# Kernel optimization log

Measured on AMD Instinct MI355X. Metric: run time of the kernel, lower is better.

## Reference

```python
import jax, jax.numpy as jnp
import numpy as np

B, T, P, D, L = 16, 120, 96, 128, 2


def setup_inputs() -> dict:
    key = jax.random.key(0)
    k1, k2, k3, k4 = jax.random.split(key, 4)
    x = jax.random.normal(k1, (B, P, D, T), dtype=jnp.float32)
    # distances: symmetric-ish positive pairwise distances from random 3D points
    pts = jax.random.uniform(k2, (B, T, P, 3), dtype=jnp.float32) * 5.0
    diff = pts[:, :, :, None, :] - pts[:, :, None, :, :]
    distances = jnp.sqrt(jnp.sum(diff * diff, axis=-1) + 1e-12)
    # contiguous-prefix padding mask (matches the original self-loop loop semantics)
    counts = jax.random.randint(k3, (B,), P // 2, P + 1)
    padding_mask = jnp.arange(P)[None, :] < counts[:, None]
    # params: xavier_uniform with gain 1e-5 ~ tiny; bias 0; LN gamma=1, beta=0
    limit = 1e-5 * np.sqrt(6.0 / (D + D))
    W = jax.random.uniform(k4, (L, D, D), minval=-limit, maxval=limit, dtype=jnp.float32)
    b = jnp.zeros((L, D), dtype=jnp.float32)
    gamma = jnp.ones((L, D), dtype=jnp.float32)
    beta = jnp.zeros((L, D), dtype=jnp.float32)
    return {"x": x, "distances": distances, "padding_mask": padding_mask,
            "W": W, "b": b, "gamma": gamma, "beta": beta}


def _build_adjacency(distances, padding_mask):
    # valid_mask: [B,T,P,P]
    vm2d = (padding_mask[:, :, None] & padding_mask[:, None, :]).astype(distances.dtype)  # [B,P,P]
    vm = vm2d[:, None, :, :]
    vd = distances * vm
    pos = (vd > 0).astype(distances.dtype)
    n = jnp.sum(pos)
    mean = jnp.sum(vd * pos) / n
    var = jnp.sum(((vd - mean) ** 2) * pos) / (n - 1.0)  # unbiased, as torch.std
    sigma = jnp.sqrt(var) + 1e-8
    adj = jnp.exp(-(distances ** 2) / (2.0 * sigma ** 2)) * vm
    # self loops on valid (contiguous-prefix) nodes: add diag(mask)
    eye_mask = jnp.eye(P, dtype=distances.dtype)[None, :, :] * padding_mask[:, :, None].astype(distances.dtype)
    adj = adj + eye_mask[:, None, :, :]
    # symmetric normalization D^{-1/2} A D^{-1/2}
    deg = jnp.clip(jnp.sum(adj, axis=-1, keepdims=True), 1e-8, None)  # [B,T,P,1]
    deg = jnp.clip(deg * padding_mask[:, None, :, None].astype(distances.dtype), 1e-8, None)
    dis = deg ** -0.5
    adj = dis * adj * jnp.swapaxes(dis, -2, -1)
    return adj * vm


def _layer_norm_D(x, g, bt, eps=1e-5):
    # x: [B,P,D,T]; normalize over D axis
    mu = jnp.mean(x, axis=2, keepdims=True)
    var = jnp.mean((x - mu) ** 2, axis=2, keepdims=True)
    return (x - mu) * jax.lax.rsqrt(var + eps) * g[None, None, :, None] + bt[None, None, :, None]


def reference(x, distances, padding_mask, W, b, gamma, beta):
    adj = _build_adjacency(distances, padding_mask)  # [B,T,P,P]
    mask_f = padding_mask.astype(x.dtype)
    for l in range(L):
        xt = jnp.transpose(x, (0, 3, 1, 2))                      # [B,T,P,D]
        h = jnp.einsum('btpd,de->btpe', xt, W[l])                # x @ W
        o = jnp.einsum('btpq,btqd->btpd', adj, h)                # A @ xW
        o = jax.nn.relu(o + b[l])
        o = o * mask_f[:, None, :, None]
        o = jnp.transpose(o, (0, 2, 3, 1))                       # [B,P,D,T]
        o = _layer_norm_D(o, gamma[l], beta[l])
        x = x + o
    return x
```

## Files before the change

kernel.cpp:

```cpp
#include <hip/hip_runtime.h>
#include <math.h>

typedef __bf16 bf16_t;
typedef __bf16 bf16x8 __attribute__((ext_vector_type(8)));
typedef __bf16 bf16x4 __attribute__((ext_vector_type(4)));
typedef float f32x4 __attribute__((ext_vector_type(4)));

namespace {
constexpr int kB = 16;
constexpr int kT = 120;
constexpr int kP = 96;
constexpr int kD = 128;
constexpr int kBT = kB * kT;
constexpr int kPP = kP * kP;
constexpr int kPD = kP * kD;
constexpr long long kND = (long long)kBT * kPP;
constexpr unsigned kND4 = (unsigned)(kND / 4);

constexpr int PREP_BLOCKS = 128;
constexpr int TIN_TILES = (kPD / 64) * kB;
constexpr int TILES_PER_BLOCK = 3;
constexpr int TIN_BLOCKS = TIN_TILES / TILES_PER_BLOCK;
constexpr int STATS_BLOCKS = 2048;
constexpr int FRONT_BLOCKS = PREP_BLOCKS + TIN_BLOCKS + STATS_BLOCKS;

constexpr int YS = 136;
constexpr int HS = 104;
constexpr int OS = 132;
constexpr int AS = 104;
constexpr int HT_OFF = 26112;
constexpr int AL_OFF = 52736;
constexpr int MROW_OFF = 72704;
constexpr int DIS_OFF = 73088;
constexpr int SMEM_B = 73472;
}

__device__ __forceinline__ f32x4 mfma16(bf16x8 a, bf16x8 b, f32x4 c) {
    return __builtin_amdgcn_mfma_f32_16x16x32_bf16(a, b, c, 0, 0, 0);
}

__global__ __launch_bounds__(256) void k_front(const float* __restrict__ x,
                                               bf16_t* __restrict__ y,
                                               const float* __restrict__ dist,
                                               const unsigned char* __restrict__ mraw,
                                               int* __restrict__ mask,
                                               double* __restrict__ stats,
                                               const float* __restrict__ W,
                                               bf16_t* __restrict__ wT) {
    __shared__ __align__(16) char sm[30976];
    const int bid = blockIdx.x;
    const int tid = threadIdx.x;

    if (bid < PREP_BLOCKS) {
        int pb = bid;
        int l = pb >> 6;
        int idx = (pb & 63) * 256 + tid;
        int n = idx >> 7, k = idx & 127;
        wT[l * 16384 + n * 128 + k] = (bf16_t)W[l * 16384 + k * 128 + n];

        if (pb == 0) {
            const unsigned int* u32 = (const unsigned int*)mraw;
            unsigned int w0 = u32[0];
            int mode;
            if (w0 == 0x01010101u) mode = 0;
            else if (w0 == 1u) mode = 1;
            else mode = 2;
            for (int i = tid; i < kB * kP; i += 256) {
                int v;
                if (mode == 0)      v = (mraw[i] != 0);
                else if (mode == 1) v = (u32[i] != 0);
                else                v = (((const float*)mraw)[i] != 0.0f);
                mask[i] = v;
            }
        }
    } else if (bid < PREP_BLOCKS + TIN_BLOCKS) {
        float* tile = (float*)sm;
        int tb = bid - PREP_BLOCKS;
        int tile0 = tb * TILES_PER_BLOCK;

        float4 pf[8];
        {
            const float* xb = x + (long long)tile0 * 7680;
            #pragma unroll
            for (int k = 0; k < 8; ++k) {
                int idx = k * 256 + tid;
                if (idx < 1920) pf[k] = *(const float4*)(xb + idx * 4);
            }
        }

        for (int it = 0; it < TILES_PER_BLOCK; ++it) {
            int tg = tile0 + it;
            #pragma unroll
            for (int k = 0; k < 8; ++k) {
                int idx = k * 256 + tid;
                if (idx < 1920) {
                    int r = idx / 30, c = (idx - r * 30) * 4;
                    tile[r * 121 + c + 0] = pf[k].x;
                    tile[r * 121 + c + 1] = pf[k].y;
                    tile[r * 121 + c + 2] = pf[k].z;
                    tile[r * 121 + c + 3] = pf[k].w;
                }
            }
            __syncthreads();
            if (it + 1 < TILES_PER_BLOCK) {
                const float* xb = x + (long long)(tg + 1) * 7680;
                #pragma unroll
                for (int k = 0; k < 8; ++k) {
                    int idx = k * 256 + tid;
                    if (idx < 1920) pf[k] = *(const float4*)(xb + idx * 4);
                }
            }
            int b = tg / (kPD / 64);
            int pd0 = (tg - b * (kPD / 64)) * 64;
            bf16_t* yb = y + (long long)b * kT * kPD + pd0;
            #pragma unroll
            for (int k = 0; k < 4; ++k) {
                int idx = k * 256 + tid;
                if (idx < 960) {
                    int t = idx >> 3, dg = idx & 7;
                    bf16x8 o;
                    #pragma unroll
                    for (int j = 0; j < 8; ++j) o[j] = (bf16_t)tile[(dg * 8 + j) * 121 + t];
                    *(bf16x8*)(yb + (long long)t * kPD + dg * 8) = o;
                }
            }
            __syncthreads();
        }
    } else {
        int sb = bid - PREP_BLOCKS - TIN_BLOCKS;
        int* ml = (int*)sm;
        double* sh = (double*)(sm + 6144);
        {
            const unsigned int* u32 = (const unsigned int*)mraw;
            unsigned int w0 = u32[0];
            int mode;
            if (w0 == 0x01010101u) mode = 0;
            else if (w0 == 1u) mode = 1;
            else mode = 2;
            for (int i = tid; i < kB * kP; i += 256) {
                int v;
                if (mode == 0)      v = (mraw[i] != 0);
                else if (mode == 1) v = (u32[i] != 0);
                else                v = (((const float*)mraw)[i] != 0.0f);
                ml[i] = v;
            }
        }
        __syncthreads();

        unsigned stride = (unsigned)STATS_BLOCKS * 256u;
        double s = 0.0, s2 = 0.0;
        int cnt = 0;
        for (unsigned i4 = (unsigned)sb * 256u + (unsigned)tid; i4 < kND4; i4 += stride) {
            unsigned q0 = (i4 % 24u) * 4u;
            unsigned r = i4 / 24u;
            unsigned p = r % 96u;
            unsigned b = r / (96u * 120u);
            const int* mb = ml + b * kP;
            if (mb[p]) {
                float4 d4 = *(const float4*)(dist + (size_t)i4 * 4);
                if (mb[q0 + 0]) { s += d4.x; s2 += (double)d4.x * d4.x; cnt++; }
                if (mb[q0 + 1]) { s += d4.y; s2 += (double)d4.y * d4.y; cnt++; }
                if (mb[q0 + 2]) { s += d4.z; s2 += (double)d4.z * d4.z; cnt++; }
                if (mb[q0 + 3]) { s += d4.w; s2 += (double)d4.w * d4.w; cnt++; }
            }
        }
        sh[tid] = s; __syncthreads();
        for (int off = 128; off > 0; off >>= 1) { if (tid < off) sh[tid] += sh[tid + off]; __syncthreads(); }
        if (tid == 0) atomicAdd(&stats[0], sh[0]);
        __syncthreads();
        sh[tid] = s2; __syncthreads();
        for (int off = 128; off > 0; off >>= 1) { if (tid < off) sh[tid] += sh[tid + off]; __syncthreads(); }
        if (tid == 0) atomicAdd(&stats[1], sh[0]);
        __syncthreads();
        sh[tid] = (double)cnt; __syncthreads();
        for (int off = 128; off > 0; off >>= 1) { if (tid < off) sh[tid] += sh[tid + off]; __syncthreads(); }
        if (tid == 0) atomicAdd(&stats[2], sh[0]);
    }
}

__global__ __launch_bounds__(256) void k_tout(const bf16_t* __restrict__ y,
                                              float* __restrict__ out) {
    __shared__ float tile[64 * 121];
    int b = blockIdx.y, pd0 = blockIdx.x * 64;
    int tid = threadIdx.x;
    const bf16_t* yb = y + (long long)b * kT * kPD + pd0;
    #pragma unroll
    for (int k = 0; k < 4; ++k) {
        int idx = k * 256 + tid;
        if (idx < 960) {
            int t = idx >> 3, dg = idx & 7;
            bf16x8 v = *(const bf16x8*)(yb + (long long)t * kPD + dg * 8);
            #pragma unroll
            for (int j = 0; j < 8; ++j) tile[(dg * 8 + j) * 121 + t] = (float)v[j];
        }
    }
    __syncthreads();
    float* ob = out + ((long long)b * kPD + pd0) * kT;
    #pragma unroll
    for (int k = 0; k < 8; ++k) {
        int idx = k * 256 + tid;
        if (idx < 1920) {
            int r = idx / 30, c = idx - r * 30;
            float4 v;
            v.x = tile[r * 121 + c * 4 + 0];
            v.y = tile[r * 121 + c * 4 + 1];
            v.z = tile[r * 121 + c * 4 + 2];
            v.w = tile[r * 121 + c * 4 + 3];
            *(float4*)(ob + r * kT + c * 4) = v;
        }
    }
}

__global__ __launch_bounds__(512, 2) void k_gcn(bf16_t* __restrict__ y,
                                                const float* __restrict__ dist,
                                                const int* __restrict__ mask,
                                                const double* __restrict__ stats,
                                                const bf16_t* __restrict__ wT,
                                                const float* __restrict__ bias,
                                                const float* __restrict__ gamma,
                                                const float* __restrict__ beta) {
    __shared__ __align__(16) char smem[SMEM_B];
    bf16_t* yL  = (bf16_t*)smem;
    bf16_t* hT  = (bf16_t*)(smem + HT_OFF);
    bf16_t* oLb = (bf16_t*)(smem + HT_OFF);
    float*  aT  = (float*)smem;
    bf16_t* aL  = (bf16_t*)(smem + AL_OFF);
    float* mrowf = (float*)(smem + MROW_OFF);
    float* dis   = (float*)(smem + DIS_OFF);

    const int tid = threadIdx.x;
    const int tx = tid & 15, ty = tid >> 4;
    const int lane = tid & 63, w = tid >> 6;
    const int wm = w >> 2, wn = w & 3;
    const int fc = lane & 15, fg = lane >> 4;
    const int bt = blockIdx.x, b = bt / kT;
    const int d0 = tx * 8;

    bf16_t* ybt = y + (size_t)bt * kPD;
    const float* dbt = dist + (size_t)bt * kPP;

    if (tid < kP) mrowf[tid] = (float)mask[b * kP + tid];

    double sn = stats[2];
    double mean = stats[0] / sn;
    double var = (stats[1] - sn * mean * mean) / (sn - 1.0);
    double sg = sqrt(var) + 1e-8;
    float inv2s2 = (float)(1.0 / (2.0 * sg * sg));

    __syncthreads();

    #pragma unroll
    for (int k = 0; k < 5; ++k) {
        int i4 = k * 512 + tid;
        if (i4 < 2304) {
            int e = i4 * 4;
            int p = e / kP, q = e - p * kP;
            float4 d4 = *(const float4*)(dbt + e);
            float mp = mrowf[p];
            float vv[4];
            vv[0] = (mp * mrowf[q + 0] != 0.f) ? __expf(-d4.x * d4.x * inv2s2) : 0.f;
            vv[1] = (mp * mrowf[q + 1] != 0.f) ? __expf(-d4.y * d4.y * inv2s2) : 0.f;
            vv[2] = (mp * mrowf[q + 2] != 0.f) ? __expf(-d4.z * d4.z * inv2s2) : 0.f;
            vv[3] = (mp * mrowf[q + 3] != 0.f) ? __expf(-d4.w * d4.w * inv2s2) : 0.f;
            #pragma unroll
            for (int j = 0; j < 4; ++j) {
                if (p == q + j) vv[j] += mp;
                aT[p * 100 + q + j] = vv[j];
            }
        }
    }
    __syncthreads();

    if (tid < kP) {
        float s = 0.f;
        for (int q = 0; q < kP; ++q) s += aT[q * 100 + tid];
        s = fmaxf(s, 1e-8f);
        s = fmaxf(s * mrowf[tid], 1e-8f);
        dis[tid] = rsqrtf(s);
    }
    __syncthreads();

    #pragma unroll
    for (int k = 0; k < 5; ++k) {
        int i4 = k * 512 + tid;
        if (i4 < 2304) {
            int e = i4 * 4;
            int p = e / kP, q = e - p * kP;
            float dp = dis[p];
            bf16x4 ov;
            #pragma unroll
            for (int j = 0; j < 4; ++j)
                ov[j] = (bf16_t)(dp * aT[p * 100 + q + j] * dis[q + j]);
            *(bf16x4*)(aL + p * AS + q) = ov;
        }
    }
    __syncthreads();

    #pragma unroll
    for (int i = 0; i < 3; ++i) {
        int p = ty * 3 + i;
        *(bf16x8*)(yL + p * YS + d0) = *(const bf16x8*)(ybt + p * kD + d0);
    }

    for (int l = 0; l < 2; ++l) {
        const bf16_t* wTl = wT + l * kD * kD;
        bf16x8 wf[4][2];
        #pragma unroll
        for (int kt = 0; kt < 4; ++kt) {
            wf[kt][0] = *(const bf16x8*)(wTl + ((wn * 2 + 0) * 16 + fc) * kD + kt * 32 + fg * 8);
            wf[kt][1] = *(const bf16x8*)(wTl + ((wn * 2 + 1) * 16 + fc) * kD + kt * 32 + fg * 8);
        }
        __syncthreads();

        f32x4 acc[3][2];
        #pragma unroll
        for (int mt = 0; mt < 3; ++mt) { acc[mt][0] = {0,0,0,0}; acc[mt][1] = {0,0,0,0}; }
        #pragma unroll
        for (int kt = 0; kt < 4; ++kt) {
            #pragma unroll
            for (int mt = 0; mt < 3; ++mt) {
                bf16x8 af = *(const bf16x8*)(yL + ((wm * 3 + mt) * 16 + fc) * YS + kt * 32 + fg * 8);
                acc[mt][0] = mfma16(af, wf[kt][0], acc[mt][0]);
                acc[mt][1] = mfma16(af, wf[kt][1], acc[mt][1]);
            }
        }
        #pragma unroll
        for (int mt = 0; mt < 3; ++mt)
            #pragma unroll
            for (int nn = 0; nn < 2; ++nn) {
                int e = (wn * 2 + nn) * 16 + fc;
                int p0 = (wm * 3 + mt) * 16 + fg * 4;
                bf16x4 hv = {(bf16_t)acc[mt][nn][0], (bf16_t)acc[mt][nn][1],
                             (bf16_t)acc[mt][nn][2], (bf16_t)acc[mt][nn][3]};
                *(bf16x4*)(hT + e * HS + p0) = hv;
            }
        __syncthreads();

        f32x4 acc2[3][2];
        #pragma unroll
        for (int mt = 0; mt < 3; ++mt) { acc2[mt][0] = {0,0,0,0}; acc2[mt][1] = {0,0,0,0}; }
        #pragma unroll
        for (int kt = 0; kt < 3; ++kt) {
            bf16x8 bf0 = *(const bf16x8*)(hT + ((wn * 2 + 0) * 16 + fc) * HS + kt * 32 + fg * 8);
            bf16x8 bf1 = *(const bf16x8*)(hT + ((wn * 2 + 1) * 16 + fc) * HS + kt * 32 + fg * 8);
            #pragma unroll
            for (int mt = 0; mt < 3; ++mt) {
                bf16x8 af = *(const bf16x8*)(aL + ((wm * 3 + mt) * 16 + fc) * AS + kt * 32 + fg * 8);
                acc2[mt][0] = mfma16(af, bf0, acc2[mt][0]);
                acc2[mt][1] = mfma16(af, bf1, acc2[mt][1]);
            }
        }
        __syncthreads();

        #pragma unroll
        for (int mt = 0; mt < 3; ++mt)
            #pragma unroll
            for (int nn = 0; nn < 2; ++nn) {
                int d = (wn * 2 + nn) * 16 + fc;
                int p0 = (wm * 3 + mt) * 16 + fg * 4;
                oLb[(p0 + 0) * OS + d] = (bf16_t)acc2[mt][nn][0];
                oLb[(p0 + 1) * OS + d] = (bf16_t)acc2[mt][nn][1];
                oLb[(p0 + 2) * OS + d] = (bf16_t)acc2[mt][nn][2];
                oLb[(p0 + 3) * OS + d] = (bf16_t)acc2[mt][nn][3];
            }
        __syncthreads();

        const float* bl = bias + l * kD;
        const float* gl = gamma + l * kD;
        const float* bel = beta + l * kD;
        float4 bb0 = *(const float4*)(bl + d0), bb1 = *(const float4*)(bl + d0 + 4);
        float4 gg0 = *(const float4*)(gl + d0), gg1 = *(const float4*)(gl + d0 + 4);
        float4 be0 = *(const float4*)(bel + d0), be1 = *(const float4*)(bel + d0 + 4);
        float bb[8] = {bb0.x, bb0.y, bb0.z, bb0.w, bb1.x, bb1.y, bb1.z, bb1.w};
        float gg[8] = {gg0.x, gg0.y, gg0.z, gg0.w, gg1.x, gg1.y, gg1.z, gg1.w};
        float be[8] = {be0.x, be0.y, be0.z, be0.w, be1.x, be1.y, be1.z, be1.w};

        #pragma unroll
        for (int i = 0; i < 3; ++i) {
            int p = ty * 3 + i;
            float mpf = mrowf[p];
            bf16x4 o0 = *(const bf16x4*)(oLb + p * OS + d0);
            bf16x4 o1 = *(const bf16x4*)(oLb + p * OS + d0 + 4);
            bf16x8 yv = *(const bf16x8*)(yL + p * YS + d0);
            float v[8];
            #pragma unroll
            for (int j = 0; j < 4; ++j) {
                v[j]     = fmaxf((float)o0[j] + bb[j], 0.f) * mpf;
                v[j + 4] = fmaxf((float)o1[j] + bb[j + 4], 0.f) * mpf;
            }
            float s = v[0] + v[1] + v[2] + v[3] + v[4] + v[5] + v[6] + v[7];
            s += __shfl_xor(s, 8);
            s += __shfl_xor(s, 4);
            s += __shfl_xor(s, 2);
            s += __shfl_xor(s, 1);
            float mu = s * 0.0078125f;

            float ss = 0.f;
            #pragma unroll
            for (int j = 0; j < 8; ++j) { float dv = v[j] - mu; ss += dv * dv; }
            ss += __shfl_xor(ss, 8);
            ss += __shfl_xor(ss, 4);
            ss += __shfl_xor(ss, 2);
            ss += __shfl_xor(ss, 1);
            float inv = rsqrtf(ss * 0.0078125f + 1e-5f);

            bf16x8 c;
            #pragma unroll
            for (int j = 0; j < 8; ++j)
                c[j] = (bf16_t)((float)yv[j] + (v[j] - mu) * inv * gg[j] + be[j]);

            if (l == 0) {
                *(bf16x8*)(yL + p * YS + d0) = c;
            } else {
                *(bf16x8*)(ybt + p * kD + d0) = c;
            }
        }
    }
}

extern "C" void kernel_launch(void* const* d_in, const int* in_sizes, int n_in,
                              void* d_out, int out_size, void* d_ws, size_t ws_size,
                              hipStream_t stream) {
    (void)in_sizes; (void)n_in; (void)out_size; (void)ws_size;

    const float* x = (const float*)d_in[0];
    const float* dist = (const float*)d_in[1];
    const unsigned char* mraw = (const unsigned char*)d_in[2];
    const float* W = (const float*)d_in[3];
    const float* bias = (const float*)d_in[4];
    const float* gamma = (const float*)d_in[5];
    const float* beta = (const float*)d_in[6];
    float* out = (float*)d_out;

    char* ws = (char*)d_ws;
    double* stats = (double*)ws;
    int* mask = (int*)(ws + 64);
    bf16_t* wT = (bf16_t*)(ws + 8192);
    bf16_t* y = (bf16_t*)(ws + 81920);

    hipMemsetAsync(stats, 0, 32, stream);

    k_front<<<FRONT_BLOCKS, 256, 0, stream>>>(x, y, dist, mraw, mask, stats, W, wT);

    k_gcn<<<kBT, 512, 0, stream>>>(y, dist, mask, stats, wT, bias, gamma, beta);

    k_tout<<<dim3(kPD / 64, kB), 256, 0, stream>>>(y, out);
}
```

Baseline: 207.4 us.

## Reorder front-kernel block roles, prefetch distance loads, use lightweight barriers

Moves the transpose-in blocks to the front of the grid so they are scheduled first, and raises tiles per block from 3 to 4. Replaces __syncthreads with a barrier that waits only on LDS counters, so in-flight global prefetches are not drained at each barrier. Software-pipelines the distance-statistics loop by loading the next float4 before processing the current one. Unconditional prefetching raises memory traffic for masked rows that were skipped before, and adds register pressure.

```diff
diff --git a/kernel.cpp b/kernel.cpp
--- a/kernel.cpp
+++ b/kernel.cpp
@@ -17,12 +17,12 @@
 constexpr long long kND = (long long)kBT * kPP;
 constexpr unsigned kND4 = (unsigned)(kND / 4);
 
+constexpr int TILES_PER_BLOCK = 4;
+constexpr int TIN_TILES = (kPD / 64) * kB;
+constexpr int TIN_BLOCKS = TIN_TILES / TILES_PER_BLOCK;
 constexpr int PREP_BLOCKS = 128;
-constexpr int TIN_TILES = (kPD / 64) * kB;
-constexpr int TILES_PER_BLOCK = 3;
-constexpr int TIN_BLOCKS = TIN_TILES / TILES_PER_BLOCK;
 constexpr int STATS_BLOCKS = 2048;
-constexpr int FRONT_BLOCKS = PREP_BLOCKS + TIN_BLOCKS + STATS_BLOCKS;
+constexpr int FRONT_BLOCKS = TIN_BLOCKS + PREP_BLOCKS + STATS_BLOCKS;
 
 constexpr int YS = 136;
 constexpr int HS = 104;
@@ -37,6 +37,12 @@
 
 __device__ __forceinline__ f32x4 mfma16(bf16x8 a, bf16x8 b, f32x4 c) {
     return __builtin_amdgcn_mfma_f32_16x16x32_bf16(a, b, c, 0, 0, 0);
+}
+
+__device__ __forceinline__ void bar_lgkm() {
+    asm volatile("s_waitcnt lgkmcnt(0)" ::: "memory");
+    __builtin_amdgcn_s_barrier();
+    __builtin_amdgcn_sched_barrier(0);
 }
 
 __global__ __launch_bounds__(256) void k_front(const float* __restrict__ x,
@@ -51,8 +57,62 @@
     const int bid = blockIdx.x;
     const int tid = threadIdx.x;
 
-    if (bid < PREP_BLOCKS) {
-        int pb = bid;
+    if (bid < TIN_BLOCKS) {
+        float* tile = (float*)sm;
+        int tile0 = bid * TILES_PER_BLOCK;
+
+        float4 pf[8];
+        {
+            const float* xb = x + (long long)tile0 * 7680;
+            #pragma unroll
+            for (int k = 0; k < 8; ++k) {
+                int idx = k * 256 + tid;
+                if (idx < 1920) pf[k] = *(const float4*)(xb + idx * 4);
+            }
+        }
+
+        for (int it = 0; it < TILES_PER_BLOCK; ++it) {
+            int tg = tile0 + it;
+            #pragma unroll
+            for (int k = 0; k < 8; ++k) {
+                int idx = k * 256 + tid;
+                if (idx < 1920) {
+                    int r = idx / 30, c = (idx - r * 30) * 4;
+                    tile[r * 121 + c + 0] = pf[k].x;
+                    tile[r * 121 + c + 1] = pf[k].y;
+                    tile[r * 121 + c + 2] = pf[k].z;
+                    tile[r * 121 + c + 3] = pf[k].w;
+                }
+            }
+            bar_lgkm();
+
+            if (it + 1 < TILES_PER_BLOCK) {
+                const float* xb = x + (long long)(tg + 1) * 7680;
+                #pragma unroll
+                for (int k = 0; k < 8; ++k) {
+                    int idx = k * 256 + tid;
+                    if (idx < 1920) pf[k] = *(const float4*)(xb + idx * 4);
+                }
+            }
+
+            int b = tg / 192;
+            int pd0 = (tg - b * 192) * 64;
+            bf16_t* yb = y + (long long)b * kT * kPD + pd0;
+            #pragma unroll
+            for (int k = 0; k < 4; ++k) {
+                int idx = k * 256 + tid;
+                if (idx < 960) {
+                    int t = idx >> 3, dg = idx & 7;
+                    bf16x8 o;
+                    #pragma unroll
+                    for (int j = 0; j < 8; ++j) o[j] = (bf16_t)tile[(dg * 8 + j) * 121 + t];
+                    *(bf16x8*)(yb + (long long)t * kPD + dg * 8) = o;
+                }
+            }
+            bar_lgkm();
+        }
+    } else if (bid < TIN_BLOCKS + PREP_BLOCKS) {
+        int pb = bid - TIN_BLOCKS;
         int l = pb >> 6;
         int idx = (pb & 63) * 256 + tid;
         int n = idx >> 7, k = idx & 127;
@@ -73,61 +133,8 @@
                 mask[i] = v;
             }
         }
-    } else if (bid < PREP_BLOCKS + TIN_BLOCKS) {
-        float* tile = (float*)sm;
-        int tb = bid - PREP_BLOCKS;
-        int tile0 = tb * TILES_PER_BLOCK;
-
-        float4 pf[8];
-        {
-            const float* xb = x + (long long)tile0 * 7680;
-            #pragma unroll
-            for (int k = 0; k < 8; ++k) {
-                int idx = k * 256 + tid;
-                if (idx < 1920) pf[k] = *(const float4*)(xb + idx * 4);
-            }
-        }
-
-        for (int it = 0; it < TILES_PER_BLOCK; ++it) {
-            int tg = tile0 + it;
-            #pragma unroll
-            for (int k = 0; k < 8; ++k) {
-                int idx = k * 256 + tid;
-                if (idx < 1920) {
-                    int r = idx / 30, c = (idx - r * 30) * 4;
-                    tile[r * 121 + c + 0] = pf[k].x;
-                    tile[r * 121 + c + 1] = pf[k].y;
-                    tile[r * 121 + c + 2] = pf[k].z;
-                    tile[r * 121 + c + 3] = pf[k].w;
-                }
-            }
-            __syncthreads();
-            if (it + 1 < TILES_PER_BLOCK) {
-                const float* xb = x + (long long)(tg + 1) * 7680;
-                #pragma unroll
-                for (int k = 0; k < 8; ++k) {
-                    int idx = k * 256 + tid;
-                    if (idx < 1920) pf[k] = *(const float4*)(xb + idx * 4);
-                }
-            }
-            int b = tg / (kPD / 64);
-            int pd0 = (tg - b * (kPD / 64)) * 64;
-            bf16_t* yb = y + (long long)b * kT * kPD + pd0;
-            #pragma unroll
-            for (int k = 0; k < 4; ++k) {
-                int idx = k * 256 + tid;
-                if (idx < 960) {
-                    int t = idx >> 3, dg = idx & 7;
-                    bf16x8 o;
-                    #pragma unroll
-                    for (int j = 0; j < 8; ++j) o[j] = (bf16_t)tile[(dg * 8 + j) * 121 + t];
-                    *(bf16x8*)(yb + (long long)t * kPD + dg * 8) = o;
-                }
-            }
-            __syncthreads();
-        }
     } else {
-        int sb = bid - PREP_BLOCKS - TIN_BLOCKS;
+        int sb = bid - TIN_BLOCKS - PREP_BLOCKS;
         int* ml = (int*)sm;
         double* sh = (double*)(sm + 6144);
         {
@@ -150,19 +157,27 @@
         unsigned stride = (unsigned)STATS_BLOCKS * 256u;
         double s = 0.0, s2 = 0.0;
         int cnt = 0;
-        for (unsigned i4 = (unsigned)sb * 256u + (unsigned)tid; i4 < kND4; i4 += stride) {
+        unsigned i4 = (unsigned)sb * 256u + (unsigned)tid;
+        bool have = i4 < kND4;
+        float4 cur = make_float4(0.f, 0.f, 0.f, 0.f);
+        if (have) cur = *(const float4*)(dist + (size_t)i4 * 4);
+        while (have) {
+            unsigned nxt = i4 + stride;
+            bool hn = nxt < kND4;
+            float4 nx = cur;
+            if (hn) nx = *(const float4*)(dist + (size_t)nxt * 4);
             unsigned q0 = (i4 % 24u) * 4u;
             unsigned r = i4 / 24u;
             unsigned p = r % 96u;
-            unsigned b = r / (96u * 120u);
+            unsigned b = r / 11520u;
             const int* mb = ml + b * kP;
             if (mb[p]) {
-                float4 d4 = *(const float4*)(dist + (size_t)i4 * 4);
-                if (mb[q0 + 0]) { s += d4.x; s2 += (double)d4.x * d4.x; cnt++; }
-                if (mb[q0 + 1]) { s += d4.y; s2 += (double)d4.y * d4.y; cnt++; }
-                if (mb[q0 + 2]) { s += d4.z; s2 += (double)d4.z * d4.z; cnt++; }
-                if (mb[q0 + 3]) { s += d4.w; s2 += (double)d4.w * d4.w; cnt++; }
-            }
+                if (mb[q0 + 0]) { s += cur.x; s2 += (double)cur.x * cur.x; cnt++; }
+                if (mb[q0 + 1]) { s += cur.y; s2 += (double)cur.y * cur.y; cnt++; }
+                if (mb[q0 + 2]) { s += cur.z; s2 += (double)cur.z * cur.z; cnt++; }
+                if (mb[q0 + 3]) { s += cur.w; s2 += (double)cur.w * cur.w; cnt++; }
+            }
+            i4 = nxt; cur = nx; have = hn;
         }
         sh[tid] = s; __syncthreads();
         for (int off = 128; off > 0; off >>= 1) { if (tid < off) sh[tid] += sh[tid + off]; __syncthreads(); }
```

Result: no change. 206.3 us (-0.5%).
